# Performance work log

Measured on AMD Instinct MI355X. Metric: run time of the kernel, lower is better.

The kernel has to match this reference:

```python
import jax, jax.numpy as jnp
import numpy as np

NUM_HEADS = 20
MAX_SEQLEN = 1500  # max per-segment length (Whisper 30s -> 1500 frames); static for jit
NEG = -1e30


def setup_inputs() -> dict:
    key = jax.random.key(0)
    ks = jax.random.split(key, 6)
    B, S, D = 4, MAX_SEQLEN, 1280
    T = B * S
    hidden_states = jax.random.normal(ks[0], (T, D), dtype=jnp.float32)
    # packed varlen layout: 4 equal-length audio segments
    cu_seqlens = (jnp.arange(B + 1, dtype=jnp.int32) * S)
    w = 0.02
    Wq = jax.random.normal(ks[1], (D, D), dtype=jnp.float32) * w
    Wk = jax.random.normal(ks[2], (D, D), dtype=jnp.float32) * w
    Wv = jax.random.normal(ks[3], (D, D), dtype=jnp.float32) * w
    Wo = jax.random.normal(ks[4], (D, D), dtype=jnp.float32) * w
    bq = jnp.zeros((D,), jnp.float32)
    bv = jnp.zeros((D,), jnp.float32)
    bo = jnp.zeros((D,), jnp.float32)
    return {"hidden_states": hidden_states, "cu_seqlens": cu_seqlens,
            "Wq": Wq, "bq": bq, "Wk": Wk, "Wv": Wv, "bv": bv, "Wo": Wo, "bo": bo}


def _varlen_attention(hidden_states, cu_seqlens, Wq, bq, Wk, Wv, bv, Wo, bo):
    T, D = hidden_states.shape
    H = NUM_HEADS
    d = D // H
    scale = d ** -0.5
    S = MAX_SEQLEN
    B = cu_seqlens.shape[0] - 1

    # projections (torch nn.Linear convention: y = x @ W.T + b; k_proj has no bias)
    q = hidden_states @ Wq.T + bq   # [T, D]
    k = hidden_states @ Wk.T        # [T, D]
    v = hidden_states @ Wv.T + bv   # [T, D]

    lens = cu_seqlens[1:] - cu_seqlens[:-1]                 # [B]
    pos = jnp.arange(S, dtype=jnp.int32)                    # [S]
    valid = pos[None, :] < lens[:, None]                    # [B, S]
    idx = cu_seqlens[:-1, None] + pos[None, :]              # [B, S]
    idx_g = jnp.where(valid, idx, 0)

    # unpack to padded [B, S, H, d]
    qb = q[idx_g].reshape(B, S, H, d)
    kb = k[idx_g].reshape(B, S, H, d)
    vb = v[idx_g].reshape(B, S, H, d)

    scores = jnp.einsum('bqhd,bkhd->bhqk', qb, kb) * scale  # [B, H, S, S]
    scores = jnp.where(valid[:, None, None, :], scores, NEG)
    attn = jax.nn.softmax(scores, axis=-1)
    out = jnp.einsum('bhqk,bkhd->bqhd', attn, vb).reshape(B, S, D)

    # repack to [T, D]; invalid slots scatter out-of-bounds and are dropped
    idx_s = jnp.where(valid, idx, T).reshape(-1)
    packed = jnp.zeros((T, D), out.dtype).at[idx_s].set(out.reshape(-1, D), mode='drop')
    return packed @ Wo.T + bo


def reference(hidden_states, cu_seqlens, Wq, bq, Wk, Wv, bv, Wo, bo):
    return _varlen_attention(hidden_states, cu_seqlens, Wq, bq, Wk, Wv, bv, Wo, bo)
```

## Files before the change

### kernel.cpp

```cpp
#include <hip/hip_runtime.h>
#include <stdint.h>
#include <math.h>

#define DMODEL 1280
#define NHEAD  20
#define DHEAD  64
#define NSEG   4
#define MAXS   1500
#define SPAD   1536
#define TPAD   (NSEG*SPAD)
#define QT256  ((MAXS + 255) / 256)
#define BM 128
#define BN 128
#define BK 32
#define QSCALE 0.18033688011112042f
#define NEGV  -1e30f

typedef float  f32x4  __attribute__((ext_vector_type(4)));
typedef __bf16 bf16x8 __attribute__((ext_vector_type(8)));

#if __has_builtin(__builtin_amdgcn_exp2f)
#define EXP2F(x) __builtin_amdgcn_exp2f(x)
#else
#define EXP2F(x) exp2f(x)
#endif

__device__ __forceinline__ ushort f2bf(float f) {
  union { float f; uint32_t u; } a; a.f = f;
  uint32_t u = a.u;
  u += 0x7FFFu + ((u >> 16) & 1u);
  return (ushort)(u >> 16);
}

__device__ __forceinline__ void async16(const void* g, void* lds) {
  __builtin_amdgcn_global_load_lds((const __attribute__((address_space(1))) void*)g,
                                   (__attribute__((address_space(3))) void*)lds,
                                   16, 0, 0);
}

__device__ __forceinline__ int perm32(int a) {
  return ((a >> 2) & 3) * 8 + ((a >> 4) & 1) * 4 + (a & 3);
}

__global__ void __launch_bounds__(256)
cvt_all(const float* __restrict__ hs, const float* __restrict__ Wq,
        const float* __restrict__ Wk, const float* __restrict__ Wv,
        const float* __restrict__ Wo, ushort* __restrict__ dst, int nX, int DD) {
  const int i = (blockIdx.x * 256 + threadIdx.x) * 4;
  const float* src;
  if (i < nX) {
    src = hs + i;
  } else {
    int j = i - nX;
    const int z = (j >= DD) + (j >= 2 * DD) + (j >= 3 * DD);
    const float* w = (z == 0) ? Wq : (z == 1) ? Wk : (z == 2) ? Wv : Wo;
    src = w + (j - z * DD);
  }
  float4 v = *(const float4*)src;
  ushort4 o;
  o.x = f2bf(v.x); o.y = f2bf(v.y); o.z = f2bf(v.z); o.w = f2bf(v.w);
  *(ushort4*)(dst + i) = o;
}

__device__ __forceinline__ void gemm_tile_mainloop(
    const ushort* __restrict__ A, const ushort* __restrict__ W,
    int M, int m0, int n0, ushort* As, ushort* Bs, f32x4 (&acc)[4][4])
{
  const int tid  = threadIdx.x;
  const int wave = tid >> 6, lane = tid & 63;
  const int quad = lane >> 4, c16 = lane & 15;
  const int wr = (wave >> 1) * 64, wc = (wave & 1) * 64;

  const int M0 = wave * 128 + lane, M1 = M0 + 64;
  const int sr0 = M0 >> 3, pp0 = M0 & 7, p0 = pp0 ^ (sr0 & 7);
  const int sr1 = M1 >> 3, pp1 = M1 & 7, p1 = pp1 ^ (sr1 & 7);
  const int row0 = sr0 * 2 + (p0 >> 2), kc0 = (p0 & 3) << 3;
  const int row1 = sr1 * 2 + (p1 >> 2), kc1 = (p1 & 3) << 3;
  const ushort* Ap0 = A + (size_t)(m0 + row0) * DMODEL + kc0;
  const ushort* Ap1 = A + (size_t)(m0 + row1) * DMODEL + kc1;
  const ushort* Bp0 = W + (size_t)(n0 + row0) * DMODEL + kc0;
  const ushort* Bp1 = W + (size_t)(n0 + row1) * DMODEL + kc1;
  const int o0 = wave * 1024;
  const int o1 = wave * 1024 + 512;
  const int BUF = BM * BK;

  async16(Ap0, As + o0); async16(Ap1, As + o1);
  async16(Bp0, Bs + o0); async16(Bp1, Bs + o1);

  int c = 0;
  for (int k0 = 0; k0 < DMODEL; k0 += BK, c ^= 1) {
    __syncthreads();
    if (k0 + BK < DMODEL) {
      const int kn = k0 + BK;
      const int bo = (c ^ 1) * BUF;
      async16(Ap0 + kn, As + bo + o0); async16(Ap1 + kn, As + bo + o1);
      async16(Bp0 + kn, Bs + bo + o0); async16(Bp1 + kn, Bs + bo + o1);
    }
    const ushort* Ab = As + c * BUF;
    const ushort* Bb = Bs + c * BUF;
    bf16x8 a[4], b[4];
#pragma unroll
    for (int i = 0; i < 4; ++i) {
      const int row = wr + i * 16 + c16;
      const int sr = row >> 1;
      const int off = (sr << 6) + (((((row & 1) << 2) | quad) ^ (sr & 7)) << 3);
      a[i] = *(const bf16x8*)(Ab + off);
    }
#pragma unroll
    for (int j = 0; j < 4; ++j) {
      const int row = wc + j * 16 + c16;
      const int sr = row >> 1;
      const int off = (sr << 6) + (((((row & 1) << 2) | quad) ^ (sr & 7)) << 3);
      b[j] = *(const bf16x8*)(Bb + off);
    }
#pragma unroll
    for (int i = 0; i < 4; ++i)
#pragma unroll
      for (int j = 0; j < 4; ++j)
        acc[i][j] = __builtin_amdgcn_mfma_f32_16x16x32_bf16(a[i], b[j], acc[i][j], 0, 0, 0);
  }
}

__global__ void __launch_bounds__(256, 4)
gemm_qkv(const ushort* __restrict__ X, const ushort* __restrict__ W4,
         const float* __restrict__ bq, const float* __restrict__ bv,
         const int* __restrict__ cu,
         ushort* __restrict__ qb, ushort* __restrict__ kb, ushort* __restrict__ vt, int M)
{
  __shared__ ushort As[2 * BM * BK], Bs[2 * BN * BK];
  const int wg = blockIdx.x;
  if (wg >= 30) return;
  const int z = wg / 10;
  const int n0 = (wg % 10) * BN;
  const int m0 = blockIdx.y * BM;
  const ushort* W = W4 + (size_t)z * DMODEL * DMODEL;

  f32x4 acc[4][4];
  f32x4 zero = {0.f, 0.f, 0.f, 0.f};
#pragma unroll
  for (int i = 0; i < 4; ++i)
#pragma unroll
    for (int j = 0; j < 4; ++j) acc[i][j] = zero;

  gemm_tile_mainloop(X, W, M, m0, n0, As, Bs, acc);

  const int tid = threadIdx.x, wave = tid >> 6, lane = tid & 63;
  const int quad = lane >> 4, c16 = lane & 15;
  const int wr = (wave >> 1) * 64, wc = (wave & 1) * 64;

  if (z == 2) {
    const int c1 = cu[1], c2 = cu[2], c3 = cu[3];
#pragma unroll
    for (int i = 0; i < 4; ++i) {
      const int t0 = m0 + wr + i * 16 + quad * 4;
      const int s0a = (t0 >= c1) + (t0 >= c2) + (t0 >= c3);
      const int s3a = (t0 + 3 >= c1) + (t0 + 3 >= c2) + (t0 + 3 >= c3);
      const int seg0 = (s0a == 0) ? 0 : (s0a == 1) ? c1 : (s0a == 2) ? c2 : c3;
#pragma unroll
      for (int j = 0; j < 4; ++j) {
        const int cfeat = n0 + wc + j * 16 + c16;
        const float bb = bv[cfeat];
        if (t0 + 3 < M && s0a == s3a) {
          const int s = t0 - seg0;
          const size_t base = (size_t)cfeat * TPAD + (size_t)s0a * SPAD
                            + (size_t)(s & ~31) + perm32(s & 31);
          ushort4 w;
          w.x = f2bf(acc[i][j][0] + bb);
          w.y = f2bf(acc[i][j][1] + bb);
          w.z = f2bf(acc[i][j][2] + bb);
          w.w = f2bf(acc[i][j][3] + bb);
          *(ushort4*)(vt + base) = w;
        } else {
#pragma unroll
          for (int r = 0; r < 4; ++r) {
            const int t = t0 + r;
            if (t < M) {
              const int sb = (t >= c1) + (t >= c2) + (t >= c3);
              const int sg = (sb == 0) ? 0 : (sb == 1) ? c1 : (sb == 2) ? c2 : c3;
              const int s = t - sg;
              vt[(size_t)cfeat * TPAD + (size_t)sb * SPAD + (s & ~31) + perm32(s & 31)]
                  = f2bf(acc[i][j][r] + bb);
            }
          }
        }
      }
    }
  } else {
    ushort* out = (z == 0) ? qb : kb;
    const float* bias = (z == 0) ? bq : (const float*)nullptr;
    const float oscale = (z == 0) ? QSCALE : 1.0f;
#pragma unroll
    for (int i = 0; i < 4; ++i) {
      const int rbase = m0 + wr + i * 16 + quad * 4;
#pragma unroll
      for (int j = 0; j < 4; ++j) {
        const int c = n0 + wc + j * 16 + c16;
        const float bb = bias ? bias[c] : 0.f;
#pragma unroll
        for (int r = 0; r < 4; ++r) {
          const int rr = rbase + r;
          if (rr < M) out[(size_t)rr * DMODEL + c] = f2bf((acc[i][j][r] + bb) * oscale);
        }
      }
    }
  }
}

__global__ void __launch_bounds__(256, 4)
gemm_out(const ushort* __restrict__ A, const ushort* __restrict__ W,
         const float* __restrict__ bias, float* __restrict__ out, int M)
{
  __shared__ ushort As[2 * BM * BK], Bs[2 * BN * BK];
  const int wg = blockIdx.x;
  if (wg >= 10) return;
  const int n0 = wg * BN;
  const int m0 = blockIdx.y * BM;
  f32x4 acc[4][4];
  f32x4 zero = {0.f, 0.f, 0.f, 0.f};
#pragma unroll
  for (int i = 0; i < 4; ++i)
#pragma unroll
    for (int j = 0; j < 4; ++j) acc[i][j] = zero;

  gemm_tile_mainloop(A, W, M, m0, n0, As, Bs, acc);

  const int tid = threadIdx.x, wave = tid >> 6, lane = tid & 63;
  const int quad = lane >> 4, c16 = lane & 15;
  const int wr = (wave >> 1) * 64, wc = (wave & 1) * 64;
#pragma unroll
  for (int i = 0; i < 4; ++i) {
    const int rbase = m0 + wr + i * 16 + quad * 4;
#pragma unroll
    for (int j = 0; j < 4; ++j) {
      const int c = n0 + wc + j * 16 + c16;
      const float bb = bias[c];
#pragma unroll
      for (int r = 0; r < 4; ++r) {
        const int rr = rbase + r;
        if (rr < M) out[(size_t)rr * DMODEL + c] = acc[i][j][r] + bb;
      }
    }
  }
}

__global__ void __launch_bounds__(512, 4)
attn_fused(const ushort* __restrict__ qb, const ushort* __restrict__ kb,
           const ushort* __restrict__ vt, ushort* __restrict__ ob,
           const int* __restrict__ cu, int T)
{
  __shared__ ushort SB[16384];
  const int hs = blockIdx.x;
  const int b = hs / NHEAD, h = hs % NHEAD;
  const int seg0 = cu[b];
  const int len  = cu[b + 1] - seg0;
  const int q0 = blockIdx.y * 256;
  if (q0 >= len) return;
  const int tid = threadIdx.x, wave = tid >> 6, lane = tid & 63;
  const int quad = lane >> 4, c16 = lane & 15;

#pragma unroll
  for (int t = 0; t < 4; ++t) {
    const int slot = t * 512 + tid;
    const int r = slot >> 3, k2 = slot & 7;
    const int col = ((k2 ^ (r & 7)) << 3);
    async16(qb + (size_t)(seg0 + q0 + r) * DMODEL + h * DHEAD + col,
            &SB[(t * 512 + wave * 64) * 8]);
  }

  const int rK = tid >> 3, kK = tid & 7;
  const int colK = ((kK ^ (rK & 7)) << 3);
  const ushort* kp = kb + (size_t)(seg0 + rK) * DMODEL + h * DHEAD + colK;
  const ushort* vp = vt + (size_t)(h * DHEAD + rK) * TPAD + (size_t)b * SPAD + colK;
  const int ldsoff = wave * 512;

  __syncthreads();

  bf16x8 aq[2][2];
#pragma unroll
  for (int n = 0; n < 2; ++n)
#pragma unroll
    for (int ks = 0; ks < 2; ++ks) {
      const int row = wave * 32 + n * 16 + c16;
      aq[n][ks] = *(const bf16x8*)(&SB[row * 64 + (((ks * 4 + quad) ^ (c16 & 7)) << 3)]);
    }

  __syncthreads();

  async16(kp, &SB[ldsoff]); async16(vp, &SB[4096 + ldsoff]);
  kp += (size_t)64 * DMODEL; vp += 64;

  float l_i[2] = {0.f, 0.f};
  f32x4 o_acc[2][4];
  f32x4 zero = {0.f, 0.f, 0.f, 0.f};
#pragma unroll
  for (int n = 0; n < 2; ++n)
#pragma unroll
    for (int m = 0; m < 4; ++m) o_acc[n][m] = zero;

  const int niter = (len + 63) >> 6;
  for (int it = 0; it < niter; ++it) {
    __syncthreads();
    const ushort* Kt = &SB[(it & 1) * 8192];
    const ushort* Vt = Kt + 4096;

    if (it + 1 < niter) {
      ushort* Dst = &SB[((it + 1) & 1) * 8192];
      async16(kp, Dst + ldsoff); async16(vp, Dst + 4096 + ldsoff);
      kp += (size_t)64 * DMODEL; vp += 64;
    }

    f32x4 s[2][4];
    __builtin_amdgcn_s_setprio(1);
#pragma unroll
    for (int f = 0; f < 4; ++f) {
      const int row = f * 16 + c16;
      const int ch = c16 & 7;
      bf16x8 ak0 = *(const bf16x8*)(Kt + row * 64 + ((quad ^ ch) << 3));
      bf16x8 ak1 = *(const bf16x8*)(Kt + row * 64 + (((4 + quad) ^ ch) << 3));
#pragma unroll
      for (int n = 0; n < 2; ++n) {
        s[n][f] = zero;
        s[n][f] = __builtin_amdgcn_mfma_f32_16x16x32_bf16(ak0, aq[n][0], s[n][f], 0, 0, 0);
        s[n][f] = __builtin_amdgcn_mfma_f32_16x16x32_bf16(ak1, aq[n][1], s[n][f], 0, 0, 0);
      }
    }
    __builtin_amdgcn_s_setprio(0);

    const int kv0 = it * 64;
    if (kv0 + 64 > len) {
#pragma unroll
      for (int f = 0; f < 4; ++f) {
        const int kvb = kv0 + f * 16 + quad * 4;
#pragma unroll
        for (int r = 0; r < 4; ++r)
          if (kvb + r >= len) { s[0][f][r] = NEGV; s[1][f][r] = NEGV; }
      }
    }

#pragma unroll
    for (int n = 0; n < 2; ++n) {
      float rs = 0.f;
#pragma unroll
      for (int f = 0; f < 4; ++f)
#pragma unroll
        for (int r = 0; r < 4; ++r) {
          const float p = EXP2F(s[n][f][r]);
          s[n][f][r] = p;
          rs += p;
        }
      l_i[n] += rs;
    }

    bf16x8 bp[2][2];
#pragma unroll
    for (int n = 0; n < 2; ++n)
#pragma unroll
      for (int g = 0; g < 2; ++g) {
        bf16x8 t;
#pragma unroll
        for (int r = 0; r < 4; ++r) {
          t[r]     = (__bf16)s[n][2 * g][r];
          t[r + 4] = (__bf16)s[n][2 * g + 1][r];
        }
        bp[n][g] = t;
      }

    __builtin_amdgcn_s_setprio(1);
#pragma unroll
    for (int m = 0; m < 4; ++m) {
      const int row = m * 16 + c16;
      const int ch = c16 & 7;
      bf16x8 av0 = *(const bf16x8*)(Vt + row * 64 + ((quad ^ ch) << 3));
      bf16x8 av1 = *(const bf16x8*)(Vt + row * 64 + (((4 + quad) ^ ch) << 3));
#pragma unroll
      for (int n = 0; n < 2; ++n) {
        o_acc[n][m] = __builtin_amdgcn_mfma_f32_16x16x32_bf16(av0, bp[n][0], o_acc[n][m], 0, 0, 0);
        o_acc[n][m] = __builtin_amdgcn_mfma_f32_16x16x32_bf16(av1, bp[n][1], o_acc[n][m], 0, 0, 0);
      }
    }
    __builtin_amdgcn_s_setprio(0);
  }

#pragma unroll
  for (int n = 0; n < 2; ++n) {
    float l = l_i[n];
    l += __shfl_xor(l, 16);
    l += __shfl_xor(l, 32);
    const int q = q0 + wave * 32 + n * 16 + c16;
    if (q < len) {
      const float inv = 1.0f / l;
      const size_t base = (size_t)(seg0 + q) * DMODEL + h * DHEAD;
#pragma unroll
      for (int m = 0; m < 4; ++m) {
        ushort4 pk;
        pk.x = f2bf(o_acc[n][m][0] * inv);
        pk.y = f2bf(o_acc[n][m][1] * inv);
        pk.z = f2bf(o_acc[n][m][2] * inv);
        pk.w = f2bf(o_acc[n][m][3] * inv);
        *(ushort4*)(ob + base + m * 16 + quad * 4) = pk;
      }
    }
  }
}

extern "C" void kernel_launch(void* const* d_in, const int* in_sizes, int n_in,
                              void* d_out, int out_size, void* d_ws, size_t ws_size,
                              hipStream_t stream)
{
  (void)n_in; (void)out_size; (void)ws_size;
  const float* hs = (const float*)d_in[0];
  const int*   cu = (const int*)d_in[1];
  const float* Wq = (const float*)d_in[2];
  const float* bq = (const float*)d_in[3];
  const float* Wk = (const float*)d_in[4];
  const float* Wv = (const float*)d_in[5];
  const float* bv = (const float*)d_in[6];
  const float* Wo = (const float*)d_in[7];
  const float* bo = (const float*)d_in[8];
  float* out = (float*)d_out;
  const int T  = in_sizes[0] / DMODEL;
  const int DD = DMODEL * DMODEL;
  const int nX = T * DMODEL;

  ushort* ws  = (ushort*)d_ws;
  ushort* X   = ws;
  ushort* W4  = X + (size_t)nX;
  ushort* qb  = W4 + 4 * (size_t)DD;
  ushort* kb  = qb + (size_t)T * DMODEL;
  ushort* vt  = kb + (size_t)T * DMODEL;
  ushort* ob  = X;

  const int ncvt = nX + 4 * DD;
  cvt_all<<<(ncvt / 4 + 255) / 256, 256, 0, stream>>>(hs, Wq, Wk, Wv, Wo, ws, nX, DD);

  gemm_qkv<<<dim3(32, (T + BM - 1) / BM), 256, 0, stream>>>(
      X, W4, bq, bv, cu, qb, kb, vt, T);

  attn_fused<<<dim3(NSEG * NHEAD, QT256), 512, 0, stream>>>(qb, kb, vt, ob, cu, T);

  gemm_out<<<dim3(16, (T + BM - 1) / BM), 256, 0, stream>>>(
      ob, W4 + 3 * (size_t)DD, bo, out, T);
}
```

Baseline: 297.8 us.

## Retile output projection to 64x128 blocks and grid-stride the conversion kernel

The output projection GEMM switches from 128x128 tiles with 256 threads, where 6 of 16 column blocks exited early, to 64x128 tiles with 128 threads (two waves, each computing 64x64). It uses its own double-buffered async LDS staging loop. This doubles the number of row blocks to fill more CUs on the 6000x1280 output and removes the wasted idle blocks. Separately, the fp32-to-bf16 conversion kernel now processes 8 elements per thread in a grid-stride loop over a fixed 2048 blocks. This cuts launch size and block overhead, at the risk of lower memory-level parallelism.

```diff
diff --git a/kernel.cpp b/kernel.cpp
--- a/kernel.cpp
+++ b/kernel.cpp
@@ -13,6 +13,8 @@
 #define BM 128
 #define BN 128
 #define BK 32
+#define OBM 64
+#define OBN 128
 #define QSCALE 0.18033688011112042f
 #define NEGV  -1e30f
 
@@ -46,20 +48,27 @@
 cvt_all(const float* __restrict__ hs, const float* __restrict__ Wq,
         const float* __restrict__ Wk, const float* __restrict__ Wv,
         const float* __restrict__ Wo, ushort* __restrict__ dst, int nX, int DD) {
-  const int i = (blockIdx.x * 256 + threadIdx.x) * 4;
-  const float* src;
-  if (i < nX) {
-    src = hs + i;
-  } else {
-    int j = i - nX;
-    const int z = (j >= DD) + (j >= 2 * DD) + (j >= 3 * DD);
-    const float* w = (z == 0) ? Wq : (z == 1) ? Wk : (z == 2) ? Wv : Wo;
-    src = w + (j - z * DD);
-  }
-  float4 v = *(const float4*)src;
-  ushort4 o;
-  o.x = f2bf(v.x); o.y = f2bf(v.y); o.z = f2bf(v.z); o.w = f2bf(v.w);
-  *(ushort4*)(dst + i) = o;
+  const int ng = (nX + 4 * DD) >> 3;
+  const int stride = gridDim.x * 256;
+  for (int g = blockIdx.x * 256 + threadIdx.x; g < ng; g += stride) {
+    const int i = g << 3;
+    const float* src;
+    if (i < nX) {
+      src = hs + i;
+    } else {
+      const int j = i - nX;
+      const int z = (j >= DD) + (j >= 2 * DD) + (j >= 3 * DD);
+      const float* w = (z == 0) ? Wq : (z == 1) ? Wk : (z == 2) ? Wv : Wo;
+      src = w + (j - z * DD);
+    }
+    const float4 v0 = ((const float4*)src)[0];
+    const float4 v1 = ((const float4*)src)[1];
+    ushort4 o0, o1;
+    o0.x = f2bf(v0.x); o0.y = f2bf(v0.y); o0.z = f2bf(v0.z); o0.w = f2bf(v0.w);
+    o1.x = f2bf(v1.x); o1.y = f2bf(v1.y); o1.z = f2bf(v1.z); o1.w = f2bf(v1.w);
+    ((ushort4*)(dst + i))[0] = o0;
+    ((ushort4*)(dst + i))[1] = o1;
+  }
 }
 
 __device__ __forceinline__ void gemm_tile_mainloop(
@@ -206,15 +215,48 @@
   }
 }
 
-__global__ void __launch_bounds__(256, 4)
+__global__ void __launch_bounds__(128, 3)
 gemm_out(const ushort* __restrict__ A, const ushort* __restrict__ W,
          const float* __restrict__ bias, float* __restrict__ out, int M)
 {
-  __shared__ ushort As[2 * BM * BK], Bs[2 * BN * BK];
-  const int wg = blockIdx.x;
-  if (wg >= 10) return;
-  const int n0 = wg * BN;
-  const int m0 = blockIdx.y * BM;
+  __shared__ ushort As[2 * OBM * BK], Bs[2 * OBN * BK];
+  const int n0 = blockIdx.x * OBN;
+  const int m0 = blockIdx.y * OBM;
+  const int tid = threadIdx.x, wave = tid >> 6, lane = tid & 63;
+  const int quad = lane >> 4, c16 = lane & 15;
+
+  int rA[2], kA[2], rB[4], kB[4];
+#pragma unroll
+  for (int q = 0; q < 2; ++q) {
+    const int s = tid + q * 128;
+    const int sr = s >> 3, p = (s & 7) ^ (sr & 7);
+    rA[q] = sr * 2 + (p >> 2); kA[q] = (p & 3) << 3;
+  }
+#pragma unroll
+  for (int q = 0; q < 4; ++q) {
+    const int s = tid + q * 128;
+    const int sr = s >> 3, p = (s & 7) ^ (sr & 7);
+    rB[q] = sr * 2 + (p >> 2); kB[q] = (p & 3) << 3;
+  }
+  const ushort* ApS0 = A + (size_t)(m0 + rA[0]) * DMODEL + kA[0];
+  const ushort* ApS1 = A + (size_t)(m0 + rA[1]) * DMODEL + kA[1];
+  const ushort* BpS0 = W + (size_t)(n0 + rB[0]) * DMODEL + kB[0];
+  const ushort* BpS1 = W + (size_t)(n0 + rB[1]) * DMODEL + kB[1];
+  const ushort* BpS2 = W + (size_t)(n0 + rB[2]) * DMODEL + kB[2];
+  const ushort* BpS3 = W + (size_t)(n0 + rB[3]) * DMODEL + kB[3];
+  const int aO0 = (wave * 64) * 8,       aO1 = (128 + wave * 64) * 8;
+  const int bO0 = (wave * 64) * 8,       bO1 = (128 + wave * 64) * 8;
+  const int bO2 = (256 + wave * 64) * 8, bO3 = (384 + wave * 64) * 8;
+  const int BUFA = OBM * BK;
+  const int BUFB = OBN * BK;
+
+#define OSTAGE(c, kk) do { \
+    ushort* Ad = As + (c) * BUFA; ushort* Bd = Bs + (c) * BUFB; \
+    async16(ApS0 + (kk), Ad + aO0); async16(ApS1 + (kk), Ad + aO1); \
+    async16(BpS0 + (kk), Bd + bO0); async16(BpS1 + (kk), Bd + bO1); \
+    async16(BpS2 + (kk), Bd + bO2); async16(BpS3 + (kk), Bd + bO3); \
+  } while (0)
+
   f32x4 acc[4][4];
   f32x4 zero = {0.f, 0.f, 0.f, 0.f};
 #pragma unroll
@@ -222,22 +264,47 @@
 #pragma unroll
     for (int j = 0; j < 4; ++j) acc[i][j] = zero;
 
-  gemm_tile_mainloop(A, W, M, m0, n0, As, Bs, acc);
-
-  const int tid = threadIdx.x, wave = tid >> 6, lane = tid & 63;
-  const int quad = lane >> 4, c16 = lane & 15;
-  const int wr = (wave >> 1) * 64, wc = (wave & 1) * 64;
+  OSTAGE(0, 0);
+  int c = 0;
+  for (int k0 = 0; k0 < DMODEL; k0 += BK, c ^= 1) {
+    __syncthreads();
+    if (k0 + BK < DMODEL) OSTAGE(c ^ 1, k0 + BK);
+    const ushort* Ab = As + c * BUFA;
+    const ushort* Bb = Bs + c * BUFB;
+    bf16x8 a[4], b[4];
+#pragma unroll
+    for (int i = 0; i < 4; ++i) {
+      const int row = i * 16 + c16;
+      const int sr = row >> 1;
+      const int off = (sr << 6) + (((((row & 1) << 2) | quad) ^ (sr & 7)) << 3);
+      a[i] = *(const bf16x8*)(Ab + off);
+    }
+#pragma unroll
+    for (int j = 0; j < 4; ++j) {
+      const int row = wave * 64 + j * 16 + c16;
+      const int sr = row >> 1;
+      const int off = (sr << 6) + (((((row & 1) << 2) | quad) ^ (sr & 7)) << 3);
+      b[j] = *(const bf16x8*)(Bb + off);
+    }
+#pragma unroll
+    for (int i = 0; i < 4; ++i)
+#pragma unroll
+      for (int j = 0; j < 4; ++j)
+        acc[i][j] = __builtin_amdgcn_mfma_f32_16x16x32_bf16(a[i], b[j], acc[i][j], 0, 0, 0);
+  }
+#undef OSTAGE
+
 #pragma unroll
   for (int i = 0; i < 4; ++i) {
-    const int rbase = m0 + wr + i * 16 + quad * 4;
+    const int rbase = m0 + i * 16 + quad * 4;
 #pragma unroll
     for (int j = 0; j < 4; ++j) {
-      const int c = n0 + wc + j * 16 + c16;
-      const float bb = bias[c];
+      const int cc = n0 + wave * 64 + j * 16 + c16;
+      const float bb = bias[cc];
 #pragma unroll
       for (int r = 0; r < 4; ++r) {
         const int rr = rbase + r;
-        if (rr < M) out[(size_t)rr * DMODEL + c] = acc[i][j][r] + bb;
+        if (rr < M) out[(size_t)rr * DMODEL + cc] = acc[i][j][r] + bb;
       }
     }
   }
@@ -430,14 +497,13 @@
   ushort* vt  = kb + (size_t)T * DMODEL;
   ushort* ob  = X;
 
-  const int ncvt = nX + 4 * DD;
-  cvt_all<<<(ncvt / 4 + 255) / 256, 256, 0, stream>>>(hs, Wq, Wk, Wv, Wo, ws, nX, DD);
+  cvt_all<<<2048, 256, 0, stream>>>(hs, Wq, Wk, Wv, Wo, ws, nX, DD);
 
   gemm_qkv<<<dim3(32, (T + BM - 1) / BM), 256, 0, stream>>>(
       X, W4, bq, bv, cu, qb, kb, vt, T);
 
   attn_fused<<<dim3(NSEG * NHEAD, QT256), 512, 0, stream>>>(qb, kb, vt, ob, cu, T);
 
-  gemm_out<<<dim3(16, (T + BM - 1) / BM), 256, 0, stream>>>(
+  gemm_out<<<dim3(10, (T + OBM - 1) / OBM), 128, 0, stream>>>(
       ob, W4 + 3 * (size_t)DD, bo, out, T);
 }
```

After: 296.6 us. About the same (-0.4%).
